# Optimization experiments

Measured on AMD Instinct MI355X. Metric: run time of the kernel, lower is better.

Reference implementation:

```python
import jax, jax.numpy as jnp
import numpy as np

EPS = 1e-6
H, A, V = 4, 64, 64  # heads, attn_dim, hidden_dim


def layer_norm(x, w, b):
    mu = jnp.mean(x, axis=-1, keepdims=True)
    var = jnp.var(x, axis=-1, keepdims=True)
    return (x - mu) * jax.lax.rsqrt(var + EPS) * w + b


def setup_inputs() -> dict:
    key = jax.random.key(0)
    B, N, D = 4, 2048, 512
    lengths = np.array([2048, 1536, 1024, 1792], np.int32)
    offsets = np.concatenate([[0], np.cumsum(lengths)]).astype(np.int32)
    L = int(offsets[-1])  # 6400
    uvqk_out = (2 * V + 2 * A) * H  # 1024
    out_in = 2 * V * H + D          # concat([u, x, normed_attn])
    ks = jax.random.split(key, 4)
    return {
        "x": jax.random.normal(ks[0], (L, D), jnp.float32),
        "x_lengths": jnp.asarray(lengths),
        "x_offsets": jnp.asarray(offsets),
        "max_seq_len": N,
        "num_targets": jnp.asarray([32, 16, 8, 64], jnp.int32),
        "uvqk_weight": jax.random.normal(ks[1], (D, uvqk_out), jnp.float32) / np.float32(np.sqrt(D)),
        "uvqk_bias": jnp.zeros((uvqk_out,), jnp.float32),
        "input_norm_weight": jnp.ones((D,), jnp.float32),
        "input_norm_bias": jnp.zeros((D,), jnp.float32),
        "output_norm_weight": jnp.ones((V * H,), jnp.float32),
        "output_norm_bias": jnp.zeros((V * H,), jnp.float32),
        "output_weight": jax.random.normal(ks[2], (out_in, D), jnp.float32) / np.float32(np.sqrt(out_in)),
    }


def reference(x, x_lengths, x_offsets, max_seq_len, num_targets,
              uvqk_weight, uvqk_bias, input_norm_weight, input_norm_bias,
              output_norm_weight, output_norm_bias, output_weight):
    L, D = x.shape
    B = x_lengths.shape[0]
    N = int(max_seq_len)
    alpha = A ** -0.5

    # fused input layernorm + UVQK projection + silu
    nx = layer_norm(x, input_norm_weight, input_norm_bias)
    uvqk = jax.nn.silu(nx @ uvqk_weight + uvqk_bias)              # [L, (2V+2A)*H]
    u = uvqk[:, : V * H]                                          # [L, V*H]
    v = uvqk[:, V * H: 2 * V * H].reshape(L, H, V)
    q = uvqk[:, 2 * V * H: 2 * V * H + A * H].reshape(L, H, A)
    k = uvqk[:, 2 * V * H + A * H:].reshape(L, H, A)

    # jagged -> padded [B, N, ...]
    pos = jnp.arange(N)
    gather_idx = jnp.clip(x_offsets[:-1, None] + pos[None, :], 0, L - 1)  # [B,N]
    valid = pos[None, :] < x_lengths[:, None]                              # [B,N]
    qp = q[gather_idx] * valid[..., None, None]
    kp = k[gather_idx] * valid[..., None, None]
    vp = v[gather_idx] * valid[..., None, None]

    # target-aware causal mask: clamp ids at uih boundary; eye | dist>0
    max_ids = (x_lengths - num_targets)[:, None]        # [B,1]
    ids = jnp.minimum(pos[None, :], max_ids)            # [B,N]
    dist = ids[:, :, None] - ids[:, None, :]            # [B,N,N]
    mask = (dist > 0) | jnp.eye(N, dtype=bool)[None]
    mask = mask & valid[:, :, None] & valid[:, None, :]

    scores = jnp.einsum("bnha,bmha->bhnm", qp, kp) * alpha
    attn_w = jax.nn.silu(scores) * (1.0 / N)
    attn_w = attn_w * mask[:, None].astype(attn_w.dtype)
    attn_p = jnp.einsum("bhnm,bmhv->bnhv", attn_w, vp).reshape(B, N, H * V)

    # padded -> jagged
    tok = jnp.arange(L)
    b_of = jnp.searchsorted(x_offsets, tok, side="right") - 1
    p_of = tok - x_offsets[b_of]
    attn = attn_p[b_of, p_of]                            # [L, H*V]

    # output: norm(attn), concat [u, x, y], project, residual (dropout off / eval)
    y = layer_norm(attn, output_norm_weight, output_norm_bias)
    y = jnp.concatenate([u, x, y], axis=1)
    return x + y @ output_weight
```

## Files before the change

### kernel.cpp

```cpp
#include <hip/hip_runtime.h>
#include <math.h>

#define NSEQ 2048
#define PIT 72

typedef __attribute__((ext_vector_type(8))) short short8;
typedef __attribute__((ext_vector_type(4))) short short4v;
typedef __attribute__((ext_vector_type(4))) float f32x4;

__device__ __forceinline__ float silu_f(float z) {
    return z * __builtin_amdgcn_rcpf(1.f + __expf(-z));
}

__device__ __forceinline__ unsigned short f2bf(float f) {
    unsigned int u = __float_as_uint(f);
    u += 0x7fffu + ((u >> 16) & 1u);
    return (unsigned short)(u >> 16);
}

__device__ __forceinline__ unsigned short f2bf_fast(float f) {
    return (unsigned short)((__float_as_uint(f) + 0x8000u) >> 16);
}

__device__ __forceinline__ short8 scale8_pow2(short8 v, float s) {
    short8 r;
    #pragma unroll
    for (int i = 0; i < 8; i++) {
        float f = __uint_as_float(((unsigned int)(unsigned short)v[i]) << 16) * s;
        r[i] = (short)(unsigned short)(__float_as_uint(f) >> 16);
    }
    return r;
}

__device__ __forceinline__ void gload16(const unsigned short* g, unsigned short* l) {
    __builtin_amdgcn_global_load_lds(
        (const __attribute__((address_space(1))) unsigned short*)g,
        (__attribute__((address_space(3))) unsigned short*)l, 16, 0, 0);
}

__global__ void __launch_bounds__(256) prep_kernel(
    const float* __restrict__ W1, unsigned short* __restrict__ W1t,
    const float* __restrict__ W2, unsigned short* __restrict__ W2t,
    const float* __restrict__ x, const float* __restrict__ inw,
    const float* __restrict__ inb,
    unsigned short* __restrict__ nxb, unsigned short* __restrict__ A2)
{
    __shared__ float t[32][33];
    int id = blockIdx.x;
    int tid = threadIdx.x;
    if (id < 1024) {
        const float* W; unsigned short* Wt; int R, C, bx, by;
        if (id < 512) { W = W1; Wt = W1t; R = 512;  C = 1024; bx = id & 31; by = id >> 5; }
        else { int i2 = id - 512; W = W2; Wt = W2t; R = 1024; C = 512; bx = i2 & 15; by = i2 >> 4; }
        int r0 = by * 32, c0 = bx * 32;
        int rr = tid >> 3, cc = (tid & 7) * 4;
        float4 v = *(const float4*)(W + (size_t)(r0 + rr) * C + c0 + cc);
        t[rr][cc] = v.x; t[rr][cc + 1] = v.y; t[rr][cc + 2] = v.z; t[rr][cc + 3] = v.w;
        __syncthreads();
        int tr = tid >> 5, tc = tid & 31;
        #pragma unroll
        for (int p = 0; p < 4; p++)
            Wt[(size_t)(c0 + tr + p * 8) * R + r0 + tc] = f2bf(t[tc][tr + p * 8]);
        return;
    }
    int lane = tid & 63, wv = tid >> 6;
    int row = (id - 1024) * 4 + wv;
    int c = lane * 8;
    const float* xr = x + (size_t)row * 512 + c;
    float4 v0 = *(const float4*)xr;
    float4 v1 = *(const float4*)(xr + 4);
    float s  = v0.x + v0.y + v0.z + v0.w + v1.x + v1.y + v1.z + v1.w;
    float sq = v0.x * v0.x + v0.y * v0.y + v0.z * v0.z + v0.w * v0.w
             + v1.x * v1.x + v1.y * v1.y + v1.z * v1.z + v1.w * v1.w;
    #pragma unroll
    for (int o = 32; o > 0; o >>= 1) { s += __shfl_xor(s, o); sq += __shfl_xor(sq, o); }
    float mu = s * (1.f / 512.f);
    float var = sq * (1.f / 512.f) - mu * mu;
    float rs = rsqrtf(var + 1e-6f);
    float4 w0 = *(const float4*)(inw + c), w1 = *(const float4*)(inw + c + 4);
    float4 b0 = *(const float4*)(inb + c), b1 = *(const float4*)(inb + c + 4);
    ushort4 hn0, hn1, hx0, hx1;
    hn0.x = f2bf((v0.x - mu) * rs * w0.x + b0.x);
    hn0.y = f2bf((v0.y - mu) * rs * w0.y + b0.y);
    hn0.z = f2bf((v0.z - mu) * rs * w0.z + b0.z);
    hn0.w = f2bf((v0.w - mu) * rs * w0.w + b0.w);
    hn1.x = f2bf((v1.x - mu) * rs * w1.x + b1.x);
    hn1.y = f2bf((v1.y - mu) * rs * w1.y + b1.y);
    hn1.z = f2bf((v1.z - mu) * rs * w1.z + b1.z);
    hn1.w = f2bf((v1.w - mu) * rs * w1.w + b1.w);
    hx0.x = f2bf(v0.x); hx0.y = f2bf(v0.y); hx0.z = f2bf(v0.z); hx0.w = f2bf(v0.w);
    hx1.x = f2bf(v1.x); hx1.y = f2bf(v1.y); hx1.z = f2bf(v1.z); hx1.w = f2bf(v1.w);
    unsigned short* nr = nxb + (size_t)row * 512 + c;
    *(ushort4*)nr = hn0; *(ushort4*)(nr + 4) = hn1;
    unsigned short* ar = A2 + (size_t)row * 1024 + 256 + c;
    *(ushort4*)ar = hx0; *(ushort4*)(ar + 4) = hx1;
}

__global__ void __launch_bounds__(256) ln256_kernel(
    const float* __restrict__ a, const float* __restrict__ w,
    const float* __restrict__ b, unsigned short* __restrict__ A2)
{
    int tid = threadIdx.x, lane = tid & 63, wv = tid >> 6;
    int row = blockIdx.x * 4 + wv;
    int c = lane * 4;
    float4 v = *(const float4*)(a + (size_t)row * 256 + c);
    float s  = v.x + v.y + v.z + v.w;
    float sq = v.x * v.x + v.y * v.y + v.z * v.z + v.w * v.w;
    #pragma unroll
    for (int o = 32; o > 0; o >>= 1) { s += __shfl_xor(s, o); sq += __shfl_xor(sq, o); }
    float mu = s * (1.f / 256.f);
    float var = sq * (1.f / 256.f) - mu * mu;
    float rs = rsqrtf(var + 1e-6f);
    float4 w4 = *(const float4*)(w + c);
    float4 b4 = *(const float4*)(b + c);
    ushort4 h;
    h.x = f2bf((v.x - mu) * rs * w4.x + b4.x);
    h.y = f2bf((v.y - mu) * rs * w4.y + b4.y);
    h.z = f2bf((v.z - mu) * rs * w4.z + b4.z);
    h.w = f2bf((v.w - mu) * rs * w4.w + b4.w);
    *(ushort4*)(A2 + (size_t)row * 1024 + 768 + c) = h;
}


__global__ void __launch_bounds__(256) gemm1_mfma(
    const unsigned short* __restrict__ Ab, const unsigned short* __restrict__ Bt,
    const float* __restrict__ bias,
    unsigned short* __restrict__ A2, unsigned short* __restrict__ qkvb)
{
    constexpr int K = 512, KIT = 8;
    __shared__ unsigned short lds[16384];
    int p = blockIdx.x;
    int l = (p & 7) * 200 + (p >> 3);
    int bm = (l >> 4) * 64, bn = (l & 15) * 64;
    int tid = threadIdx.x, lane = tid & 63, w = tid >> 6;
    int wr = w >> 1, wc = w & 1;
    int nn = lane & 15, qd = lane >> 4;

    int r8 = lane >> 3, u = lane & 7;
    int su = ((u ^ r8) << 3);
    int rA0 = w * 16;
    const unsigned short* Asrc = Ab + (size_t)(bm + rA0 + r8) * K + su;
    const unsigned short* Bsrc = Bt + (size_t)(bn + rA0 + r8) * K + su;

    int fsw = nn & 7;

    f32x4 acc[2][2];
    #pragma unroll
    for (int i = 0; i < 2; i++)
        #pragma unroll
        for (int j = 0; j < 2; j++) acc[i][j] = (f32x4){0.f, 0.f, 0.f, 0.f};

    gload16(Asrc,         &lds[rA0 * 64]);
    gload16(Asrc + 8 * K, &lds[(rA0 + 8) * 64]);
    gload16(Bsrc,         &lds[4096 + rA0 * 64]);
    gload16(Bsrc + 8 * K, &lds[4096 + (rA0 + 8) * 64]);
    __syncthreads();

    for (int it = 0; it < KIT; ++it) {
        int cur = it & 1;
        unsigned short* Asc = lds + cur * 8192;
        unsigned short* Bsc = Asc + 4096;
        if (it + 1 < KIT) {
            unsigned short* An = lds + (cur ^ 1) * 8192;
            const unsigned short* a2 = Asrc + (it + 1) * 64;
            const unsigned short* b2 = Bsrc + (it + 1) * 64;
            gload16(a2,         &An[rA0 * 64]);
            gload16(a2 + 8 * K, &An[(rA0 + 8) * 64]);
            gload16(b2,         &An[4096 + rA0 * 64]);
            gload16(b2 + 8 * K, &An[4096 + (rA0 + 8) * 64]);
        }
        #pragma unroll
        for (int kk = 0; kk < 2; kk++) {
            int un = (((kk * 4 + qd) ^ fsw) << 3);
            short8 af[2], bf[2];
            #pragma unroll
            for (int i = 0; i < 2; i++)
                af[i] = *(const short8*)&Asc[(wr * 32 + i * 16 + nn) * 64 + un];
            #pragma unroll
            for (int j = 0; j < 2; j++)
                bf[j] = *(const short8*)&Bsc[(wc * 32 + j * 16 + nn) * 64 + un];
            #pragma unroll
            for (int i = 0; i < 2; i++)
                #pragma unroll
                for (int j = 0; j < 2; j++)
                    acc[i][j] = __builtin_amdgcn_mfma_f32_16x16x32_bf16(af[i], bf[j], acc[i][j], 0, 0, 0);
        }
        __syncthreads();
    }

    bool isU = (bn < 256);
    #pragma unroll
    for (int j = 0; j < 2; j++) {
        int col = bn + wc * 32 + j * 16 + nn;
        float bb = bias[col];
        #pragma unroll
        for (int i = 0; i < 2; i++) {
            int rbase = bm + wr * 32 + i * 16 + qd * 4;
            #pragma unroll
            for (int r = 0; r < 4; r++) {
                unsigned short hh = f2bf(silu_f(acc[i][j][r] + bb));
                if (isU) A2[(size_t)(rbase + r) * 1024 + col] = hh;
                else     qkvb[(size_t)(rbase + r) * 768 + col - 256] = hh;
            }
        }
    }
}

__global__ void __launch_bounds__(256) gemm2_mfma(
    const unsigned short* __restrict__ Ab, const unsigned short* __restrict__ Bt,
    const float* __restrict__ x, float* __restrict__ out)
{
    constexpr int K = 1024, KIT = 16;
    __shared__ unsigned short lds[16384];
    int p = blockIdx.x;
    int l = (p & 7) * 100 + (p >> 3);
    int bm = (l >> 3) * 64, bn = (l & 7) * 64;
    int tid = threadIdx.x, lane = tid & 63, w = tid >> 6;
    int wr = w >> 1, wc = w & 1;
    int nn = lane & 15, qd = lane >> 4;

    int r8 = lane >> 3, u = lane & 7;
    int su = ((u ^ r8) << 3);
    int rA0 = w * 16;
    const unsigned short* Asrc = Ab + (size_t)(bm + rA0 + r8) * K + su;
    const unsigned short* Bsrc = Bt + (size_t)(bn + rA0 + r8) * K + su;

    int fsw = nn & 7;

    f32x4 acc[2][2];
    #pragma unroll
    for (int i = 0; i < 2; i++)
        #pragma unroll
        for (int j = 0; j < 2; j++) acc[i][j] = (f32x4){0.f, 0.f, 0.f, 0.f};

    gload16(Asrc,         &lds[rA0 * 64]);
    gload16(Asrc + 8 * K, &lds[(rA0 + 8) * 64]);
    gload16(Bsrc,         &lds[4096 + rA0 * 64]);
    gload16(Bsrc + 8 * K, &lds[4096 + (rA0 + 8) * 64]);
    __syncthreads();

    for (int it = 0; it < KIT; ++it) {
        int cur = it & 1;
        unsigned short* Asc = lds + cur * 8192;
        unsigned short* Bsc = Asc + 4096;
        if (it + 1 < KIT) {
            unsigned short* An = lds + (cur ^ 1) * 8192;
            const unsigned short* a2 = Asrc + (it + 1) * 64;
            const unsigned short* b2 = Bsrc + (it + 1) * 64;
            gload16(a2,         &An[rA0 * 64]);
            gload16(a2 + 8 * K, &An[(rA0 + 8) * 64]);
            gload16(b2,         &An[4096 + rA0 * 64]);
            gload16(b2 + 8 * K, &An[4096 + (rA0 + 8) * 64]);
        }
        #pragma unroll
        for (int kk = 0; kk < 2; kk++) {
            int un = (((kk * 4 + qd) ^ fsw) << 3);
            short8 af[2], bf[2];
            #pragma unroll
            for (int i = 0; i < 2; i++)
                af[i] = *(const short8*)&Asc[(wr * 32 + i * 16 + nn) * 64 + un];
            #pragma unroll
            for (int j = 0; j < 2; j++)
                bf[j] = *(const short8*)&Bsc[(wc * 32 + j * 16 + nn) * 64 + un];
            #pragma unroll
            for (int i = 0; i < 2; i++)
                #pragma unroll
                for (int j = 0; j < 2; j++)
                    acc[i][j] = __builtin_amdgcn_mfma_f32_16x16x32_bf16(af[i], bf[j], acc[i][j], 0, 0, 0);
        }
        __syncthreads();
    }

    #pragma unroll
    for (int j = 0; j < 2; j++) {
        int col = bn + wc * 32 + j * 16 + nn;
        #pragma unroll
        for (int i = 0; i < 2; i++) {
            int rbase = bm + wr * 32 + i * 16 + qd * 4;
            #pragma unroll
            for (int r = 0; r < 4; r++) {
                size_t idx = (size_t)(rbase + r) * 512 + col;
                out[idx] = x[idx] + acc[i][j][r];
            }
        }
    }
}

__global__ void __launch_bounds__(256, 2) attn_mfma_kernel(
    const unsigned short* __restrict__ qkvb,
    const int* __restrict__ offsets,
    const int* __restrict__ lengths,
    const int* __restrict__ num_targets,
    float* __restrict__ attn)
{
    int id = blockIdx.x;
    int bh = id & 15;
    int xt = id >> 4;
    int b = bh >> 2, h = bh & 3;
    int len = lengths[b];
    int n0 = (31 - xt) * 64;
    if (n0 >= len) return;
    int m_hi = min(n0 + 63, len - 1);
    int off = offsets[b];
    int max_id = len - num_targets[b];
    int tid = threadIdx.x, lane = tid & 63, w = tid >> 6;
    int nn = lane & 15, qd = lane >> 4;

    __shared__ __align__(16) char smem[69632];
    unsigned short* Vt = (unsigned short*)(smem + w * 9216);
    float* Os = (float*)smem;

    short8 qf[4][2];
    #pragma unroll
    for (int g = 0; g < 4; g++) {
        int row = min(n0 + g * 16 + nn, len - 1);
        const unsigned short* base = qkvb + (size_t)(off + row) * 768 + 256 + h * 64;
        qf[g][0] = scale8_pow2(*(const short8*)(base + qd * 8), 0.125f);
        qf[g][1] = scale8_pow2(*(const short8*)(base + 32 + qd * 8), 0.125f);
    }

    f32x4 o_acc[4][4];
    #pragma unroll
    for (int t = 0; t < 4; t++)
        #pragma unroll
        for (int g = 0; g < 4; g++) o_acc[t][g] = (f32x4){0.f, 0.f, 0.f, 0.f};

    int fast_lim = min(n0, max_id);
    int r0 = (lane & 15) * 4, d0 = (lane >> 4) * 16;

    short8 kf[4][2], kn[4][2], vf[4][2];
    int m_first = w * 64;
    if (m_first <= m_hi) {
        #pragma unroll
        for (int s = 0; s < 4; s++) {
            int row = min(m_first + s * 16 + nn, len - 1);
            const unsigned short* kb = qkvb + (size_t)(off + row) * 768 + 512 + h * 64 + qd * 8;
            kf[s][0] = *(const short8*)kb;
            kf[s][1] = *(const short8*)(kb + 32);
        }
        #pragma unroll
        for (int j = 0; j < 4; j++) {
            int row = min(m_first + r0 + j, len - 1);
            const unsigned short* vb = qkvb + (size_t)(off + row) * 768 + h * 64 + d0;
            vf[j][0] = *(const short8*)vb;
            vf[j][1] = *(const short8*)(vb + 8);
        }
    }

    for (int m0 = m_first; m0 <= m_hi; m0 += 256) {
        #pragma unroll
        for (int dd = 0; dd < 16; dd++) {
            int hh = dd >> 3, e = dd & 7;
            short4v pk;
            pk[0] = vf[0][hh][e]; pk[1] = vf[1][hh][e];
            pk[2] = vf[2][hh][e]; pk[3] = vf[3][hh][e];
            *(short4v*)&Vt[(d0 + dd) * PIT + r0] = pk;
        }
        int mnext = m0 + 256;
        if (mnext <= m_hi) {
            #pragma unroll
            for (int j = 0; j < 4; j++) {
                int row = min(mnext + r0 + j, len - 1);
                const unsigned short* vb = qkvb + (size_t)(off + row) * 768 + h * 64 + d0;
                vf[j][0] = *(const short8*)vb;
                vf[j][1] = *(const short8*)(vb + 8);
            }
            #pragma unroll
            for (int s = 0; s < 4; s++) {
                int row = min(mnext + s * 16 + nn, len - 1);
                const unsigned short* kb = qkvb + (size_t)(off + row) * 768 + 512 + h * 64 + qd * 8;
                kn[s][0] = *(const short8*)kb;
                kn[s][1] = *(const short8*)(kb + 32);
            }
        }
        bool fastp = (m0 + 63 < fast_lim);
        #pragma unroll
        for (int s = 0; s < 4; s++) {
            f32x4 st[4];
            __builtin_amdgcn_s_setprio(1);
            #pragma unroll
            for (int g = 0; g < 4; g++) {
                st[g] = (f32x4){0.f, 0.f, 0.f, 0.f};
                st[g] = __builtin_amdgcn_mfma_f32_16x16x32_bf16(kf[s][0], qf[g][0], st[g], 0, 0, 0);
                st[g] = __builtin_amdgcn_mfma_f32_16x16x32_bf16(kf[s][1], qf[g][1], st[g], 0, 0, 0);
            }
            __builtin_amdgcn_s_setprio(0);
            short4v bop[4];
            if (fastp) {
                #pragma unroll
                for (int g = 0; g < 4; g++)
                    #pragma unroll
                    for (int r = 0; r < 4; r++)
                        bop[g][r] = (short)f2bf_fast(silu_f(st[g][r]));
            } else {
                #pragma unroll
                for (int g = 0; g < 4; g++) {
                    int nc_ = n0 + g * 16 + nn;
                    int id_ = min(nc_, max_id);
                    #pragma unroll
                    for (int r = 0; r < 4; r++) {
                        int mcol = m0 + s * 16 + qd * 4 + r;
                        bool ok = (mcol < id_) || (mcol == nc_);
                        bop[g][r] = (short)f2bf_fast(ok ? silu_f(st[g][r]) : 0.f);
                    }
                }
            }
            __builtin_amdgcn_s_setprio(1);
            #pragma unroll
            for (int t = 0; t < 4; t++) {
                short4v aop = *(const short4v*)&Vt[(t * 16 + nn) * PIT + s * 16 + qd * 4];
                #pragma unroll
                for (int g = 0; g < 4; g++)
                    o_acc[t][g] = __builtin_amdgcn_mfma_f32_16x16x16bf16_1k(aop, bop[g], o_acc[t][g], 0, 0, 0);
            }
            __builtin_amdgcn_s_setprio(0);
        }
        if (mnext <= m_hi) {
            #pragma unroll
            for (int s = 0; s < 4; s++) { kf[s][0] = kn[s][0]; kf[s][1] = kn[s][1]; }
        }
    }

    __syncthreads();
    const float invN = 1.f / (float)NSEQ;
    float* Ow = Os + w * 4352;
    #pragma unroll
    for (int t = 0; t < 4; t++)
        #pragma unroll
        for (int g = 0; g < 4; g++) {
            f32x4 v = o_acc[t][g] * invN;
            *(f32x4*)&Ow[(g * 16 + nn) * 68 + t * 16 + qd * 4] = v;
        }
    __syncthreads();
    int rr = tid >> 2, cs = (tid & 3) * 16;
    if (n0 + rr < len) {
        float* dst = attn + (size_t)(off + n0 + rr) * 256 + h * 64 + cs;
        #pragma unroll
        for (int q4 = 0; q4 < 4; q4++) {
            f32x4 v = (f32x4){0.f, 0.f, 0.f, 0.f};
            #pragma unroll
            for (int w2 = 0; w2 < 4; w2++)
                v += *(const f32x4*)&Os[w2 * 4352 + rr * 68 + cs + q4 * 4];
            *(f32x4*)(dst + q4 * 4) = v;
        }
    }
}

extern "C" void kernel_launch(void* const* d_in, const int* in_sizes, int n_in,
                              void* d_out, int out_size, void* d_ws, size_t ws_size,
                              hipStream_t stream)
{
    const float* x          = (const float*)d_in[0];
    const int*   x_lengths  = (const int*)d_in[1];
    const int*   x_offsets  = (const int*)d_in[2];
    const int*   num_targets = (const int*)d_in[4];
    const float* uvqk_w     = (const float*)d_in[5];
    const float* uvqk_b     = (const float*)d_in[6];
    const float* in_w       = (const float*)d_in[7];
    const float* in_b       = (const float*)d_in[8];
    const float* out_w      = (const float*)d_in[9];
    const float* out_b      = (const float*)d_in[10];
    const float* Wo         = (const float*)d_in[11];
    float* out = (float*)d_out;

    int L = in_sizes[0] / 512;

    char* ws = (char*)d_ws;
    size_t o = 0;
    float* attn = (float*)(ws + o);          o += (size_t)L * 256 * 4;
    unsigned short* nxb  = (unsigned short*)(ws + o); o += (size_t)L * 512 * 2;
    unsigned short* A2   = (unsigned short*)(ws + o); o += (size_t)L * 1024 * 2;
    unsigned short* qkvb = (unsigned short*)(ws + o); o += (size_t)L * 768 * 2;
    unsigned short* W1t  = (unsigned short*)(ws + o); o += (size_t)1024 * 512 * 2;
    unsigned short* W2t  = (unsigned short*)(ws + o); o += (size_t)512 * 1024 * 2;

    prep_kernel<<<dim3(1024 + L / 4), 256, 0, stream>>>(
        uvqk_w, W1t, Wo, W2t, x, in_w, in_b, nxb, A2);

    gemm1_mfma<<<dim3(1600), 256, 0, stream>>>(nxb, W1t, uvqk_b, A2, qkvb);

    attn_mfma_kernel<<<dim3(512), 256, 0, stream>>>(qkvb, x_offsets, x_lengths, num_targets, attn);

    ln256_kernel<<<L / 4, 256, 0, stream>>>(attn, out_w, out_b, A2);

    gemm2_mfma<<<dim3(800), 256, 0, stream>>>(A2, W2t, x, out);
}
```

Baseline: 151.8 us.

## Prefetch two K-tiles ahead in GEMMs with explicit vmcnt waits

Both MFMA GEMM kernels now issue the first two K-tiles up front and, after each compute step, refill the buffer just consumed with tile it+2. A partial s_waitcnt vmcnt(4) plus a raw s_barrier replaces the full __syncthreads, so one tile's loads stay in flight while the current tile is computed. This is meant to hide global-to-LDS latency better, and launch bounds now request 5 blocks per CU. It depends on gload16 being counted by vmcnt and on the compiler not reordering around the inline waits, and it risks register pressure from the occupancy hint.

```diff
diff --git a/kernel.cpp b/kernel.cpp
--- a/kernel.cpp
+++ b/kernel.cpp
@@ -122,7 +122,7 @@
 }
 
 
-__global__ void __launch_bounds__(256) gemm1_mfma(
+__global__ void __launch_bounds__(256, 5) gemm1_mfma(
     const unsigned short* __restrict__ Ab, const unsigned short* __restrict__ Bt,
     const float* __restrict__ bias,
     unsigned short* __restrict__ A2, unsigned short* __restrict__ qkvb)
@@ -150,25 +150,22 @@
         #pragma unroll
         for (int j = 0; j < 2; j++) acc[i][j] = (f32x4){0.f, 0.f, 0.f, 0.f};
 
-    gload16(Asrc,         &lds[rA0 * 64]);
-    gload16(Asrc + 8 * K, &lds[(rA0 + 8) * 64]);
-    gload16(Bsrc,         &lds[4096 + rA0 * 64]);
-    gload16(Bsrc + 8 * K, &lds[4096 + (rA0 + 8) * 64]);
-    __syncthreads();
+    gload16(Asrc,              &lds[rA0 * 64]);
+    gload16(Asrc + 8 * K,      &lds[(rA0 + 8) * 64]);
+    gload16(Bsrc,              &lds[4096 + rA0 * 64]);
+    gload16(Bsrc + 8 * K,      &lds[4096 + (rA0 + 8) * 64]);
+    gload16(Asrc + 64,         &lds[8192 + rA0 * 64]);
+    gload16(Asrc + 8 * K + 64, &lds[8192 + (rA0 + 8) * 64]);
+    gload16(Bsrc + 64,         &lds[12288 + rA0 * 64]);
+    gload16(Bsrc + 8 * K + 64, &lds[12288 + (rA0 + 8) * 64]);
 
     for (int it = 0; it < KIT; ++it) {
         int cur = it & 1;
         unsigned short* Asc = lds + cur * 8192;
         unsigned short* Bsc = Asc + 4096;
-        if (it + 1 < KIT) {
-            unsigned short* An = lds + (cur ^ 1) * 8192;
-            const unsigned short* a2 = Asrc + (it + 1) * 64;
-            const unsigned short* b2 = Bsrc + (it + 1) * 64;
-            gload16(a2,         &An[rA0 * 64]);
-            gload16(a2 + 8 * K, &An[(rA0 + 8) * 64]);
-            gload16(b2,         &An[4096 + rA0 * 64]);
-            gload16(b2 + 8 * K, &An[4096 + (rA0 + 8) * 64]);
-        }
+        if (it == KIT - 1) asm volatile("s_waitcnt vmcnt(0)" ::: "memory");
+        else               asm volatile("s_waitcnt vmcnt(4)" ::: "memory");
+        __builtin_amdgcn_s_barrier();
         #pragma unroll
         for (int kk = 0; kk < 2; kk++) {
             int un = (((kk * 4 + qd) ^ fsw) << 3);
@@ -185,7 +182,15 @@
                 for (int j = 0; j < 2; j++)
                     acc[i][j] = __builtin_amdgcn_mfma_f32_16x16x32_bf16(af[i], bf[j], acc[i][j], 0, 0, 0);
         }
-        __syncthreads();
+        __builtin_amdgcn_s_barrier();
+        if (it + 2 < KIT) {
+            const unsigned short* a2 = Asrc + (it + 2) * 64;
+            const unsigned short* b2 = Bsrc + (it + 2) * 64;
+            gload16(a2,         &Asc[rA0 * 64]);
+            gload16(a2 + 8 * K, &Asc[(rA0 + 8) * 64]);
+            gload16(b2,         &Bsc[rA0 * 64]);
+            gload16(b2 + 8 * K, &Bsc[(rA0 + 8) * 64]);
+        }
     }
 
     bool isU = (bn < 256);
@@ -206,7 +211,7 @@
     }
 }
 
-__global__ void __launch_bounds__(256) gemm2_mfma(
+__global__ void __launch_bounds__(256, 5) gemm2_mfma(
     const unsigned short* __restrict__ Ab, const unsigned short* __restrict__ Bt,
     const float* __restrict__ x, float* __restrict__ out)
 {
@@ -233,25 +238,22 @@
         #pragma unroll
         for (int j = 0; j < 2; j++) acc[i][j] = (f32x4){0.f, 0.f, 0.f, 0.f};
 
-    gload16(Asrc,         &lds[rA0 * 64]);
-    gload16(Asrc + 8 * K, &lds[(rA0 + 8) * 64]);
-    gload16(Bsrc,         &lds[4096 + rA0 * 64]);
-    gload16(Bsrc + 8 * K, &lds[4096 + (rA0 + 8) * 64]);
-    __syncthreads();
+    gload16(Asrc,              &lds[rA0 * 64]);
+    gload16(Asrc + 8 * K,      &lds[(rA0 + 8) * 64]);
+    gload16(Bsrc,              &lds[4096 + rA0 * 64]);
+    gload16(Bsrc + 8 * K,      &lds[4096 + (rA0 + 8) * 64]);
+    gload16(Asrc + 64,         &lds[8192 + rA0 * 64]);
+    gload16(Asrc + 8 * K + 64, &lds[8192 + (rA0 + 8) * 64]);
+    gload16(Bsrc + 64,         &lds[12288 + rA0 * 64]);
+    gload16(Bsrc + 8 * K + 64, &lds[12288 + (rA0 + 8) * 64]);
 
     for (int it = 0; it < KIT; ++it) {
         int cur = it & 1;
         unsigned short* Asc = lds + cur * 8192;
         unsigned short* Bsc = Asc + 4096;
-        if (it + 1 < KIT) {
-            unsigned short* An = lds + (cur ^ 1) * 8192;
-            const unsigned short* a2 = Asrc + (it + 1) * 64;
-            const unsigned short* b2 = Bsrc + (it + 1) * 64;
-            gload16(a2,         &An[rA0 * 64]);
-            gload16(a2 + 8 * K, &An[(rA0 + 8) * 64]);
-            gload16(b2,         &An[4096 + rA0 * 64]);
-            gload16(b2 + 8 * K, &An[4096 + (rA0 + 8) * 64]);
-        }
+        if (it == KIT - 1) asm volatile("s_waitcnt vmcnt(0)" ::: "memory");
+        else               asm volatile("s_waitcnt vmcnt(4)" ::: "memory");
+        __builtin_amdgcn_s_barrier();
         #pragma unroll
         for (int kk = 0; kk < 2; kk++) {
             int un = (((kk * 4 + qd) ^ fsw) << 3);
@@ -268,7 +270,15 @@
                 for (int j = 0; j < 2; j++)
                     acc[i][j] = __builtin_amdgcn_mfma_f32_16x16x32_bf16(af[i], bf[j], acc[i][j], 0, 0, 0);
         }
-        __syncthreads();
+        __builtin_amdgcn_s_barrier();
+        if (it + 2 < KIT) {
+            const unsigned short* a2 = Asrc + (it + 2) * 64;
+            const unsigned short* b2 = Bsrc + (it + 2) * 64;
+            gload16(a2,         &Asc[rA0 * 64]);
+            gload16(a2 + 8 * K, &Asc[(rA0 + 8) * 64]);
+            gload16(b2,         &Bsc[rA0 * 64]);
+            gload16(b2 + 8 * K, &Bsc[(rA0 + 8) * 64]);
+        }
     }
 
     #pragma unroll
```

Result: no change. 150.7 us (-0.7%).
